# Performance work log

Hardware: AMD Instinct MI355X
Metric: run time of the kernel (lower is better)

The kernel has to match this reference:

```python
import jax, jax.numpy as jnp
import numpy as np

D_MODEL = 256
NHEAD = 8
D_HEAD = D_MODEL // NHEAD


def setup_inputs() -> dict:
    key = jax.random.key(0)
    ks = jax.random.split(key, 5)
    s = 0.02
    return {
        "x": jax.random.normal(ks[0], (2, 4096, D_MODEL), dtype=jnp.float32),
        "source": jax.random.normal(ks[1], (2, 6144, D_MODEL), dtype=jnp.float32),
        "Wq": jax.random.normal(ks[2], (D_MODEL, D_MODEL), dtype=jnp.float32) * s,
        "Wk": jax.random.normal(ks[3], (D_MODEL, D_MODEL), dtype=jnp.float32) * s,
        "Wv": jax.random.normal(ks[4], (D_MODEL, D_MODEL), dtype=jnp.float32) * s,
    }


def reference(x, source, Wq, Wk, Wv):
    B, L1, D = x.shape
    L2 = source.shape[1]
    scale = D_HEAD ** (-0.5)
    # torch Linear: y = x @ W.T  (W is [out, in])
    q = (x @ Wq.T).reshape(B, L1, NHEAD, D_HEAD)
    k = (source @ Wk.T).reshape(B, L2, NHEAD, D_HEAD)
    v = (source @ Wv.T).reshape(B, L2, NHEAD, D_HEAD)
    # scores: [B, H, L1, L2]
    attn = jnp.einsum("bqhd,bkhd->bhqk", q, k) * scale
    attn = jax.nn.softmax(attn, axis=-1)
    out = jnp.einsum("bhqk,bkhd->bqhd", attn, v)
    return out.reshape(B, L1, D)
```

## Files before the change

kernel.cpp:

```cpp
#include <hip/hip_runtime.h>
#include <math.h>

#define B_   2
#define L1_  4096
#define L2_  6144
#define DM_  256
#define H_   8
#define DH_  32

typedef __bf16 bf16x8 __attribute__((ext_vector_type(8)));
typedef __bf16 bf16x4 __attribute__((ext_vector_type(4)));
typedef float floatx4 __attribute__((ext_vector_type(4)));

__device__ __forceinline__ bf16x8 ldb(const __bf16* p) { return *(const bf16x8*)p; }

__device__ __forceinline__ bf16x4 pack4(floatx4 v) {
    bf16x4 r;
    r[0] = (__bf16)v[0]; r[1] = (__bf16)v[1];
    r[2] = (__bf16)v[2]; r[3] = (__bf16)v[3];
    return r;
}

__global__ __launch_bounds__(256) void cvt_all(
    const float* __restrict__ wq, const float* __restrict__ wk,
    const float* __restrict__ wv, const float* __restrict__ x,
    const float* __restrict__ src,
    __bf16* __restrict__ wbf, __bf16* __restrict__ xbf, __bf16* __restrict__ sbf,
    float qscale)
{
    int i = blockIdx.x * 256 + threadIdx.x;
    const float* s; __bf16* d; float sc = 1.0f; size_t off;
    if (i < 49152) {
        int seg = i >> 14;
        off = (size_t)(i & 16383) * 4;
        s = seg == 0 ? wq : (seg == 1 ? wk : wv);
        d = wbf + (size_t)seg * 65536;
        if (seg == 0) sc = qscale;
    } else if (i < 49152 + 524288) {
        off = (size_t)(i - 49152) * 4; s = x; d = xbf;
    } else {
        off = (size_t)(i - 49152 - 524288) * 4; s = src; d = sbf;
    }
    float4 v = *(const float4*)(s + off);
    bf16x4 r;
    r[0] = (__bf16)(v.x * sc); r[1] = (__bf16)(v.y * sc);
    r[2] = (__bf16)(v.z * sc); r[3] = (__bf16)(v.w * sc);
    *(bf16x4*)(d + off) = r;
}

__global__ __launch_bounds__(256) void proj_kernel(
    const __bf16* __restrict__ xbf, const __bf16* __restrict__ sbf,
    const __bf16* __restrict__ Wbf,
    __bf16* __restrict__ qo, __bf16* __restrict__ ko, __bf16* __restrict__ vo)
{
    __shared__ __bf16 ldsV[256 * 36];

    const int bid = blockIdx.x;
    int y, xb;
    if      (bid < 256) { y = 0; xb = bid; }
    else if (bid < 640) { y = 1; xb = bid - 256; }
    else                { y = 2; xb = bid - 640; }

    const int L = (y == 0) ? L1_ : L2_;
    const __bf16* X   = (y == 0) ? xbf : sbf;
    const __bf16* Wb  = Wbf + (size_t)y * 65536;
    __bf16*       out = (y == 0) ? qo : (y == 1 ? ko : vo);

    const int lane = threadIdx.x & 63;
    const int w    = threadIdx.x >> 6;
    const int g    = lane >> 4;
    const int c    = lane & 15;
    const int mb   = xb * 32;
    const int b    = mb / L;
    const int lb   = mb - b * L;

    floatx4 acc[2][4];
#pragma unroll
    for (int s = 0; s < 2; s++)
#pragma unroll
        for (int n = 0; n < 4; n++) acc[s][n] = (floatx4){0.f, 0.f, 0.f, 0.f};

#pragma unroll
    for (int kc = 0; kc < 8; kc++) {
        bf16x8 xf0 = ldb(X + (size_t)(mb + c) * DM_ + kc * 32 + g * 8);
        bf16x8 xf1 = ldb(X + (size_t)(mb + 16 + c) * DM_ + kc * 32 + g * 8);
#pragma unroll
        for (int n = 0; n < 4; n++) {
            const int oc = w * 64 + n * 16 + c;
            bf16x8 wf = ldb(Wb + (size_t)oc * DM_ + kc * 32 + g * 8);
            if (y == 2) {
                acc[0][n] = __builtin_amdgcn_mfma_f32_16x16x32_bf16(xf0, wf, acc[0][n], 0, 0, 0);
                acc[1][n] = __builtin_amdgcn_mfma_f32_16x16x32_bf16(xf1, wf, acc[1][n], 0, 0, 0);
            } else {
                acc[0][n] = __builtin_amdgcn_mfma_f32_16x16x32_bf16(wf, xf0, acc[0][n], 0, 0, 0);
                acc[1][n] = __builtin_amdgcn_mfma_f32_16x16x32_bf16(wf, xf1, acc[1][n], 0, 0, 0);
            }
        }
    }

    const int bhb = b * H_;
    if (y == 2) {
#pragma unroll
        for (int s = 0; s < 2; s++)
#pragma unroll
            for (int n = 0; n < 4; n++) {
                int dg = w * 64 + (n >> 1) * 32 + (n & 1) * 16 + c;
                int ll = s * 16 + g * 4;
                *(bf16x4*)(ldsV + (size_t)dg * 36 + ll) = pack4(acc[s][n]);
            }
        __syncthreads();
        const int t = threadIdx.x;
        const int h = t >> 5, d = t & 31;
        __bf16* row = out + ((size_t)(bhb + h) * DH_ + d) * (size_t)L + lb;
#pragma unroll
        for (int j = 0; j < 4; j++)
            *(bf16x8*)(row + j * 8) = *(const bf16x8*)(ldsV + (size_t)t * 36 + j * 8);
    } else {
#pragma unroll
        for (int s = 0; s < 2; s++)
#pragma unroll
            for (int n = 0; n < 4; n++) {
                int dlo = (n & 1) * 16 + g * 4;
                int h = w * 2 + (n >> 1);
                int l = lb + s * 16 + c;
                *(bf16x4*)(out + ((size_t)(bhb + h) * (size_t)L + l) * DH_ + dlo) = pack4(acc[s][n]);
            }
    }
}

__device__ __forceinline__ void attn_step(
    const bf16x8 (&qf)[4], const bf16x8 (&kf)[4], bf16x8 (&kfN)[4],
    const __bf16* __restrict__ knext,
    const __bf16* __restrict__ vb0, const __bf16* __restrict__ vb1, int kb,
    __bf16* __restrict__ Pw, int g, int c,
    float (&l)[4], floatx4 (&o)[4][2])
{
    bf16x8 vf0 = ldb(vb0 + kb);
    bf16x8 vf1 = ldb(vb1 + kb);
    bf16x8 vf2 = ldb(vb0 + kb + 32);
    bf16x8 vf3 = ldb(vb1 + kb + 32);
    kfN[0] = ldb(knext);
    kfN[1] = ldb(knext + 16 * DH_);
    kfN[2] = ldb(knext + 32 * DH_);
    kfN[3] = ldb(knext + 48 * DH_);

#pragma unroll
    for (int h = 0; h < 4; h++) {
        floatx4 s[4];
#pragma unroll
        for (int st = 0; st < 4; st++)
            s[st] = __builtin_amdgcn_mfma_f32_16x16x32_bf16(
                        kf[st], qf[h], (floatx4){0.f, 0.f, 0.f, 0.f}, 0, 0, 0);
#pragma unroll
        for (int st = 0; st < 4; st++) {
            float a0 = __builtin_amdgcn_exp2f(s[st][0]);
            float a1 = __builtin_amdgcn_exp2f(s[st][1]);
            float a2 = __builtin_amdgcn_exp2f(s[st][2]);
            float a3 = __builtin_amdgcn_exp2f(s[st][3]);
            l[h] += (a0 + a1) + (a2 + a3);
            bf16x4 pk;
            pk[0] = (__bf16)a0; pk[1] = (__bf16)a1;
            pk[2] = (__bf16)a2; pk[3] = (__bf16)a3;
            *(bf16x4*)(Pw + h * 1024 + ((st * 2 + (g >> 1)) * 16 + c) * 8 + (g & 1) * 4) = pk;
        }
    }

#pragma unroll
    for (int kc = 0; kc < 2; kc++) {
#pragma unroll
        for (int h = 0; h < 4; h++) {
            bf16x8 pa = *(const bf16x8*)(Pw + h * 1024 + ((kc * 4 + g) * 16 + c) * 8);
            o[h][0] = __builtin_amdgcn_mfma_f32_16x16x32_bf16(pa, kc ? vf2 : vf0, o[h][0], 0, 0, 0);
            o[h][1] = __builtin_amdgcn_mfma_f32_16x16x32_bf16(pa, kc ? vf3 : vf1, o[h][1], 0, 0, 0);
        }
    }
}

template<bool DIRECT>
__global__ __launch_bounds__(256, 2) void attn_kernel(
    const __bf16* __restrict__ Q, const __bf16* __restrict__ K,
    const __bf16* __restrict__ VT, float* __restrict__ out,
    float* __restrict__ Opart, float* __restrict__ Lpart, int klen, int split)
{
    __shared__ __bf16 ldsP[4][4][1024];

    const int bid  = blockIdx.x;
    const int work = (bid & 7) * (32 * split) + (bid >> 3);
    const int xb   = work & 15;
    const int bh   = (work >> 4) & 15;
    const int z    = work >> 8;

    const int lane  = threadIdx.x & 63;
    const int w     = threadIdx.x >> 6;
    const int g     = lane >> 4;
    const int c     = lane & 15;
    const int qbase = xb * 256 + w * 64;
    const int k0    = z * klen;

    bf16x8 qf[4];
#pragma unroll
    for (int h = 0; h < 4; h++)
        qf[h] = ldb(Q + ((size_t)bh * L1_ + qbase + h * 16 + c) * DH_ + g * 8);

    const __bf16* kbase = K  + (size_t)bh * L2_ * DH_ + (size_t)c * DH_ + g * 8;
    const __bf16* vb0   = VT + ((size_t)bh * DH_ + c)      * L2_ + g * 8;
    const __bf16* vb1   = VT + ((size_t)bh * DH_ + 16 + c) * L2_ + g * 8;
    __bf16* Pw = &ldsP[w][0][0];

    float l[4] = {0.f, 0.f, 0.f, 0.f};
    floatx4 o[4][2];
#pragma unroll
    for (int h = 0; h < 4; h++) { o[h][0] = (floatx4){0.f,0.f,0.f,0.f}; o[h][1] = (floatx4){0.f,0.f,0.f,0.f}; }

    bf16x8 kfA[4], kfB[4];
#pragma unroll
    for (int st = 0; st < 4; st++)
        kfA[st] = ldb(kbase + (size_t)(k0 + st * 16) * DH_);

    for (int t = 0; t < klen; t += 128) {
        int kb = k0 + t;
        attn_step(qf, kfA, kfB, kbase + (size_t)(kb + 64) * DH_,
                  vb0, vb1, kb, Pw, g, c, l, o);
        int nn = (t + 128 < klen) ? kb + 128 : k0;
        attn_step(qf, kfB, kfA, kbase + (size_t)nn * DH_,
                  vb0, vb1, kb + 64, Pw, g, c, l, o);
    }

#pragma unroll
    for (int h = 0; h < 4; h++) {
        l[h] += __shfl_xor(l[h], 16, 64);
        l[h] += __shfl_xor(l[h], 32, 64);
    }

    const int b  = bh / H_;
    const int hh = bh % H_;
    if (DIRECT) {
#pragma unroll
        for (int h = 0; h < 4; h++)
#pragma unroll
            for (int r = 0; r < 4; r++) {
                float lr  = __shfl(l[h], g * 4 + r, 64);
                float inv = 1.0f / lr;
                size_t base = ((size_t)(b * L1_ + qbase + h * 16 + g * 4 + r)) * DM_ + hh * DH_;
                out[base + c]      = o[h][0][r] * inv;
                out[base + 16 + c] = o[h][1][r] * inv;
            }
    } else {
        float* Op = Opart + (size_t)z * ((size_t)B_ * L1_ * DM_);
#pragma unroll
        for (int h = 0; h < 4; h++) {
#pragma unroll
            for (int r = 0; r < 4; r++) {
                size_t base = ((size_t)(b * L1_ + qbase + h * 16 + g * 4 + r)) * DM_ + hh * DH_;
                Op[base + c]      = o[h][0][r];
                Op[base + 16 + c] = o[h][1][r];
            }
            if (g == 0)
                Lpart[(size_t)z * ((size_t)B_ * H_ * L1_) +
                      (size_t)bh * L1_ + qbase + h * 16 + c] = l[h];
        }
    }
}

__global__ __launch_bounds__(256) void combine_kernel(
    const float* __restrict__ Opart, const float* __restrict__ Lpart,
    float* __restrict__ out, int split)
{
    int t   = blockIdx.x * 256 + threadIdx.x;
    int row = t >> 6;
    int col = (t & 63) * 4;
    int b   = row >> 12;
    int q   = row & (L1_ - 1);
    int bh  = b * H_ + (col >> 5);
    float4 a = {0.f, 0.f, 0.f, 0.f};
    float ls = 0.f;
    for (int z = 0; z < split; z++) {
        const float* Op = Opart + (size_t)z * ((size_t)B_ * L1_ * DM_);
        float4 v = *(const float4*)(Op + (size_t)row * DM_ + col);
        a.x += v.x; a.y += v.y; a.z += v.z; a.w += v.w;
        ls += Lpart[(size_t)z * ((size_t)B_ * H_ * L1_) + (size_t)bh * L1_ + q];
    }
    float inv = 1.0f / ls;
    float4 r; r.x = a.x * inv; r.y = a.y * inv; r.z = a.z * inv; r.w = a.w * inv;
    *(float4*)(out + (size_t)row * DM_ + col) = r;
}

extern "C" void kernel_launch(void* const* d_in, const int* in_sizes, int n_in,
                              void* d_out, int out_size, void* d_ws, size_t ws_size,
                              hipStream_t stream) {
    const float* x   = (const float*)d_in[0];
    const float* src = (const float*)d_in[1];
    const float* Wq  = (const float*)d_in[2];
    const float* Wk  = (const float*)d_in[3];
    const float* Wv  = (const float*)d_in[4];
    float* out = (float*)d_out;

    const float qscale = 1.4426950408889634f / sqrtf((float)DH_);

    const size_t nW = 3 * 65536;
    const size_t nQ = (size_t)B_ * H_ * L1_ * DH_;
    const size_t nK = (size_t)B_ * H_ * L2_ * DH_;
    const size_t nX = nQ;
    const size_t nS = nK;

    __bf16* wbf = (__bf16*)d_ws;
    __bf16* qws = wbf + nW;
    __bf16* kws = qws + nQ;
    __bf16* vt  = kws + nK;
    size_t unionOff = ((nW + nQ + 2 * nK) * sizeof(__bf16) + 255) & ~(size_t)255;
    __bf16* xbf = (__bf16*)((char*)d_ws + unionOff);
    __bf16* sbf = xbf + nX;

    const size_t oPartB = (size_t)B_ * L1_ * DM_ * 4;
    const size_t lPartB = (size_t)B_ * H_ * L1_ * 4;
    const size_t avail  = ws_size > unionOff ? ws_size - unionOff : 0;
    int split = 1;
    if      (avail >= 4 * (oPartB + lPartB)) split = 4;
    else if (avail >= 2 * (oPartB + lPartB)) split = 2;
    float* Opart = (float*)((char*)d_ws + unionOff);
    float* Lpart = (float*)((char*)d_ws + unionOff + (size_t)split * oPartB);

    cvt_all<<<dim3(5312), 256, 0, stream>>>(Wq, Wk, Wv, x, src, wbf, xbf, sbf, qscale);
    proj_kernel<<<dim3(1024), 256, 0, stream>>>(xbf, sbf, wbf, qws, kws, vt);

    if (split > 1) {
        attn_kernel<false><<<dim3(256 * split), 256, 0, stream>>>(
            qws, kws, vt, nullptr, Opart, Lpart, L2_ / split, split);
        combine_kernel<<<dim3(2048), 256, 0, stream>>>(Opart, Lpart, out, split);
    } else {
        attn_kernel<true><<<dim3(256), 256, 0, stream>>>(
            qws, kws, vt, out, nullptr, nullptr, L2_, 1);
    }
}
```

Measured before the change: 188.9 us.

## Use fp16 for P and V, halve P staging, fp16 partials, deeper split

Stores the transposed V projection and the softmax probabilities in fp16. P is packed with the hardware packed round-toward-zero convert instead of per-element bf16 rounding, and the PV product uses the f16 MFMA. The attention step now processes heads in pairs, so the per-wave LDS P buffer shrinks from four heads to two. Split-K partial outputs are stored in fp16 to cut combine traffic, and the split factor may rise to 6 or 8 when workspace allows. The risks are fp16 range or precision limits on the unnormalized partial sums, and extra combine and launch work at higher split.

```diff
diff --git a/kernel.cpp b/kernel.cpp
--- a/kernel.cpp
+++ b/kernel.cpp
@@ -11,6 +11,10 @@
 typedef __bf16 bf16x8 __attribute__((ext_vector_type(8)));
 typedef __bf16 bf16x4 __attribute__((ext_vector_type(4)));
 typedef float floatx4 __attribute__((ext_vector_type(4)));
+typedef _Float16 f16;
+typedef _Float16 f16x4 __attribute__((ext_vector_type(4)));
+typedef _Float16 f16x8 __attribute__((ext_vector_type(8)));
+typedef __fp16 fp16v2 __attribute__((ext_vector_type(2)));
 
 __device__ __forceinline__ bf16x8 ldb(const __bf16* p) { return *(const bf16x8*)p; }
 
@@ -19,6 +23,11 @@
     r[0] = (__bf16)v[0]; r[1] = (__bf16)v[1];
     r[2] = (__bf16)v[2]; r[3] = (__bf16)v[3];
     return r;
+}
+
+__device__ __forceinline__ float pkrtz(float a, float b) {
+    fp16v2 p = __builtin_amdgcn_cvt_pkrtz(a, b);
+    return __builtin_bit_cast(float, p);
 }
 
 __global__ __launch_bounds__(256) void cvt_all(
@@ -51,9 +60,9 @@
 __global__ __launch_bounds__(256) void proj_kernel(
     const __bf16* __restrict__ xbf, const __bf16* __restrict__ sbf,
     const __bf16* __restrict__ Wbf,
-    __bf16* __restrict__ qo, __bf16* __restrict__ ko, __bf16* __restrict__ vo)
-{
-    __shared__ __bf16 ldsV[256 * 36];
+    __bf16* __restrict__ qo, __bf16* __restrict__ ko, f16* __restrict__ vo)
+{
+    __shared__ f16 ldsV[256 * 36];
 
     const int bid = blockIdx.x;
     int y, xb;
@@ -64,7 +73,6 @@
     const int L = (y == 0) ? L1_ : L2_;
     const __bf16* X   = (y == 0) ? xbf : sbf;
     const __bf16* Wb  = Wbf + (size_t)y * 65536;
-    __bf16*       out = (y == 0) ? qo : (y == 1 ? ko : vo);
 
     const int lane = threadIdx.x & 63;
     const int w    = threadIdx.x >> 6;
@@ -106,16 +114,20 @@
             for (int n = 0; n < 4; n++) {
                 int dg = w * 64 + (n >> 1) * 32 + (n & 1) * 16 + c;
                 int ll = s * 16 + g * 4;
-                *(bf16x4*)(ldsV + (size_t)dg * 36 + ll) = pack4(acc[s][n]);
+                float2 pr;
+                pr.x = pkrtz(acc[s][n][0], acc[s][n][1]);
+                pr.y = pkrtz(acc[s][n][2], acc[s][n][3]);
+                *(float2*)(ldsV + (size_t)dg * 36 + ll) = pr;
             }
         __syncthreads();
         const int t = threadIdx.x;
         const int h = t >> 5, d = t & 31;
-        __bf16* row = out + ((size_t)(bhb + h) * DH_ + d) * (size_t)L + lb;
-#pragma unroll
-        for (int j = 0; j < 4; j++)
-            *(bf16x8*)(row + j * 8) = *(const bf16x8*)(ldsV + (size_t)t * 36 + j * 8);
+        f16* row = vo + ((size_t)(bhb + h) * DH_ + d) * (size_t)L + lb;
+#pragma unroll
+        for (int j = 0; j < 8; j++)
+            *(f16x4*)(row + j * 4) = *(const f16x4*)(ldsV + (size_t)t * 36 + j * 4);
     } else {
+        __bf16* out = (y == 0) ? qo : ko;
 #pragma unroll
         for (int s = 0; s < 2; s++)
 #pragma unroll
@@ -131,58 +143,62 @@
 __device__ __forceinline__ void attn_step(
     const bf16x8 (&qf)[4], const bf16x8 (&kf)[4], bf16x8 (&kfN)[4],
     const __bf16* __restrict__ knext,
-    const __bf16* __restrict__ vb0, const __bf16* __restrict__ vb1, int kb,
-    __bf16* __restrict__ Pw, int g, int c,
+    const f16* __restrict__ vb0, const f16* __restrict__ vb1, int kb,
+    f16* __restrict__ Pw, int g, int c,
     float (&l)[4], floatx4 (&o)[4][2])
 {
-    bf16x8 vf0 = ldb(vb0 + kb);
-    bf16x8 vf1 = ldb(vb1 + kb);
-    bf16x8 vf2 = ldb(vb0 + kb + 32);
-    bf16x8 vf3 = ldb(vb1 + kb + 32);
+    f16x8 vf[4];
+    vf[0] = *(const f16x8*)(vb0 + kb);
+    vf[1] = *(const f16x8*)(vb1 + kb);
+    vf[2] = *(const f16x8*)(vb0 + kb + 32);
+    vf[3] = *(const f16x8*)(vb1 + kb + 32);
     kfN[0] = ldb(knext);
     kfN[1] = ldb(knext + 16 * DH_);
     kfN[2] = ldb(knext + 32 * DH_);
     kfN[3] = ldb(knext + 48 * DH_);
 
 #pragma unroll
-    for (int h = 0; h < 4; h++) {
-        floatx4 s[4];
-#pragma unroll
-        for (int st = 0; st < 4; st++)
-            s[st] = __builtin_amdgcn_mfma_f32_16x16x32_bf16(
-                        kf[st], qf[h], (floatx4){0.f, 0.f, 0.f, 0.f}, 0, 0, 0);
-#pragma unroll
-        for (int st = 0; st < 4; st++) {
-            float a0 = __builtin_amdgcn_exp2f(s[st][0]);
-            float a1 = __builtin_amdgcn_exp2f(s[st][1]);
-            float a2 = __builtin_amdgcn_exp2f(s[st][2]);
-            float a3 = __builtin_amdgcn_exp2f(s[st][3]);
-            l[h] += (a0 + a1) + (a2 + a3);
-            bf16x4 pk;
-            pk[0] = (__bf16)a0; pk[1] = (__bf16)a1;
-            pk[2] = (__bf16)a2; pk[3] = (__bf16)a3;
-            *(bf16x4*)(Pw + h * 1024 + ((st * 2 + (g >> 1)) * 16 + c) * 8 + (g & 1) * 4) = pk;
+    for (int hp = 0; hp < 2; hp++) {
+#pragma unroll
+        for (int hh = 0; hh < 2; hh++) {
+            const int h = hp * 2 + hh;
+            floatx4 s[4];
+#pragma unroll
+            for (int st = 0; st < 4; st++)
+                s[st] = __builtin_amdgcn_mfma_f32_16x16x32_bf16(
+                            kf[st], qf[h], (floatx4){0.f, 0.f, 0.f, 0.f}, 0, 0, 0);
+#pragma unroll
+            for (int st = 0; st < 4; st++) {
+                float e0 = __builtin_amdgcn_exp2f(s[st][0]);
+                float e1 = __builtin_amdgcn_exp2f(s[st][1]);
+                float e2 = __builtin_amdgcn_exp2f(s[st][2]);
+                float e3 = __builtin_amdgcn_exp2f(s[st][3]);
+                l[h] += (e0 + e1) + (e2 + e3);
+                float2 pr;
+                pr.x = pkrtz(e0, e1);
+                pr.y = pkrtz(e2, e3);
+                *(float2*)(Pw + hh * 1024 + ((st * 2 + (g >> 1)) * 16 + c) * 8 + (g & 1) * 4) = pr;
+            }
         }
-    }
-
-#pragma unroll
-    for (int kc = 0; kc < 2; kc++) {
-#pragma unroll
-        for (int h = 0; h < 4; h++) {
-            bf16x8 pa = *(const bf16x8*)(Pw + h * 1024 + ((kc * 4 + g) * 16 + c) * 8);
-            o[h][0] = __builtin_amdgcn_mfma_f32_16x16x32_bf16(pa, kc ? vf2 : vf0, o[h][0], 0, 0, 0);
-            o[h][1] = __builtin_amdgcn_mfma_f32_16x16x32_bf16(pa, kc ? vf3 : vf1, o[h][1], 0, 0, 0);
-        }
+#pragma unroll
+        for (int kc = 0; kc < 2; kc++)
+#pragma unroll
+            for (int hh = 0; hh < 2; hh++) {
+                const int h = hp * 2 + hh;
+                f16x8 pa = *(const f16x8*)(Pw + hh * 1024 + ((kc * 4 + g) * 16 + c) * 8);
+                o[h][0] = __builtin_amdgcn_mfma_f32_16x16x32_f16(pa, vf[kc * 2 + 0], o[h][0], 0, 0, 0);
+                o[h][1] = __builtin_amdgcn_mfma_f32_16x16x32_f16(pa, vf[kc * 2 + 1], o[h][1], 0, 0, 0);
+            }
     }
 }
 
 template<bool DIRECT>
 __global__ __launch_bounds__(256, 2) void attn_kernel(
     const __bf16* __restrict__ Q, const __bf16* __restrict__ K,
-    const __bf16* __restrict__ VT, float* __restrict__ out,
-    float* __restrict__ Opart, float* __restrict__ Lpart, int klen, int split)
-{
-    __shared__ __bf16 ldsP[4][4][1024];
+    const f16* __restrict__ VT, float* __restrict__ out,
+    f16* __restrict__ Opart, float* __restrict__ Lpart, int klen, int split)
+{
+    __shared__ f16 ldsP[4][2][1024];
 
     const int bid  = blockIdx.x;
     const int work = (bid & 7) * (32 * split) + (bid >> 3);
@@ -203,9 +219,9 @@
         qf[h] = ldb(Q + ((size_t)bh * L1_ + qbase + h * 16 + c) * DH_ + g * 8);
 
     const __bf16* kbase = K  + (size_t)bh * L2_ * DH_ + (size_t)c * DH_ + g * 8;
-    const __bf16* vb0   = VT + ((size_t)bh * DH_ + c)      * L2_ + g * 8;
-    const __bf16* vb1   = VT + ((size_t)bh * DH_ + 16 + c) * L2_ + g * 8;
-    __bf16* Pw = &ldsP[w][0][0];
+    const f16*    vb0   = VT + ((size_t)bh * DH_ + c)      * L2_ + g * 8;
+    const f16*    vb1   = VT + ((size_t)bh * DH_ + 16 + c) * L2_ + g * 8;
+    f16* Pw = &ldsP[w][0][0];
 
     float l[4] = {0.f, 0.f, 0.f, 0.f};
     floatx4 o[4][2];
@@ -246,14 +262,14 @@
                 out[base + 16 + c] = o[h][1][r] * inv;
             }
     } else {
-        float* Op = Opart + (size_t)z * ((size_t)B_ * L1_ * DM_);
+        f16* Op = Opart + (size_t)z * ((size_t)B_ * L1_ * DM_);
 #pragma unroll
         for (int h = 0; h < 4; h++) {
 #pragma unroll
             for (int r = 0; r < 4; r++) {
                 size_t base = ((size_t)(b * L1_ + qbase + h * 16 + g * 4 + r)) * DM_ + hh * DH_;
-                Op[base + c]      = o[h][0][r];
-                Op[base + 16 + c] = o[h][1][r];
+                Op[base + c]      = (f16)o[h][0][r];
+                Op[base + 16 + c] = (f16)o[h][1][r];
             }
             if (g == 0)
                 Lpart[(size_t)z * ((size_t)B_ * H_ * L1_) +
@@ -263,7 +279,7 @@
 }
 
 __global__ __launch_bounds__(256) void combine_kernel(
-    const float* __restrict__ Opart, const float* __restrict__ Lpart,
+    const f16* __restrict__ Opart, const float* __restrict__ Lpart,
     float* __restrict__ out, int split)
 {
     int t   = blockIdx.x * 256 + threadIdx.x;
@@ -275,9 +291,10 @@
     float4 a = {0.f, 0.f, 0.f, 0.f};
     float ls = 0.f;
     for (int z = 0; z < split; z++) {
-        const float* Op = Opart + (size_t)z * ((size_t)B_ * L1_ * DM_);
-        float4 v = *(const float4*)(Op + (size_t)row * DM_ + col);
-        a.x += v.x; a.y += v.y; a.z += v.z; a.w += v.w;
+        const f16* Op = Opart + (size_t)z * ((size_t)B_ * L1_ * DM_);
+        f16x4 v = *(const f16x4*)(Op + (size_t)row * DM_ + col);
+        a.x += (float)v[0]; a.y += (float)v[1];
+        a.z += (float)v[2]; a.w += (float)v[3];
         ls += Lpart[(size_t)z * ((size_t)B_ * H_ * L1_) + (size_t)bh * L1_ + q];
     }
     float inv = 1.0f / ls;
@@ -301,23 +318,24 @@
     const size_t nQ = (size_t)B_ * H_ * L1_ * DH_;
     const size_t nK = (size_t)B_ * H_ * L2_ * DH_;
     const size_t nX = nQ;
-    const size_t nS = nK;
 
     __bf16* wbf = (__bf16*)d_ws;
     __bf16* qws = wbf + nW;
     __bf16* kws = qws + nQ;
-    __bf16* vt  = kws + nK;
-    size_t unionOff = ((nW + nQ + 2 * nK) * sizeof(__bf16) + 255) & ~(size_t)255;
+    f16*    vt  = (f16*)(kws + nK);
+    size_t unionOff = ((nW + nQ + 2 * nK) * 2 + 255) & ~(size_t)255;
     __bf16* xbf = (__bf16*)((char*)d_ws + unionOff);
     __bf16* sbf = xbf + nX;
 
-    const size_t oPartB = (size_t)B_ * L1_ * DM_ * 4;
+    const size_t oPartB = (size_t)B_ * L1_ * DM_ * sizeof(f16);
     const size_t lPartB = (size_t)B_ * H_ * L1_ * 4;
     const size_t avail  = ws_size > unionOff ? ws_size - unionOff : 0;
     int split = 1;
-    if      (avail >= 4 * (oPartB + lPartB)) split = 4;
+    if      (avail >= 8 * (oPartB + lPartB)) split = 8;
+    else if (avail >= 6 * (oPartB + lPartB)) split = 6;
+    else if (avail >= 4 * (oPartB + lPartB)) split = 4;
     else if (avail >= 2 * (oPartB + lPartB)) split = 2;
-    float* Opart = (float*)((char*)d_ws + unionOff);
+    f16*   Opart = (f16*)((char*)d_ws + unionOff);
     float* Lpart = (float*)((char*)d_ws + unionOff + (size_t)split * oPartB);
 
     cvt_all<<<dim3(5312), 256, 0, stream>>>(Wq, Wk, Wv, x, src, wbf, xbf, sbf, qscale);
```

Result: no change. 188.8 us (-0.0%).
